# Performance work log

Measured on AMD Instinct MI355X. Metric: run time of the kernel, lower is better.

Reference implementation:

```python
import jax, jax.numpy as jnp
import numpy as np

B, T, D, H, O = 8, 16384, 256, 256, 256


def setup_inputs() -> dict:
    key = jax.random.key(0)
    ks = jax.random.split(key, 7)
    lim_d = 1.0 / np.sqrt(D)
    lim_h = 1.0 / np.sqrt(H)
    u = lambda k, shape, lim: jax.random.uniform(k, shape, jnp.float32, -lim, lim)
    return {
        "xs": jax.random.normal(ks[0], (B, T, D), jnp.float32),
        "Wz": u(ks[1], (H, D), lim_d),
        "bz": u(ks[2], (H,), lim_d),
        "Wh": u(ks[3], (H, D), lim_d),
        "bh": u(ks[4], (H,), lim_d),
        "Wo": u(ks[5], (O, H), lim_h),
        "bo": u(ks[6], (O,), lim_h),
    }


def reference(xs, Wz, bz, Wh, bh, Wo, bo):
    # gates and candidate hidden states (eqx.nn.Linear: y = W @ x + b)
    zs = jax.nn.sigmoid(jnp.einsum("btd,hd->bth", xs, Wz) + bz)  # [B,T,H]
    hs = jnp.einsum("btd,hd->bth", xs, Wh) + bh                  # [B,T,H]

    # prepend_ones / prepend_zeros along the time axis
    a = jnp.concatenate([jnp.ones_like(zs[:, :1]), 1.0 - zs], axis=1)    # [B,T+1,H]
    b = jnp.concatenate([jnp.zeros_like(zs[:, :1]), zs * hs], axis=1)    # [B,T+1,H]

    def combine(first, second):
        a0, b0 = first
        a1, b1 = second
        return (a0 * b0, b0 * a1 + b1)

    _, states = jax.lax.associative_scan(combine, (a, b), axis=1)
    return jnp.einsum("bth,oh->bto", states[:, 1:], Wo) + bo  # [B,T,O]
```

## Files before the change

### kernel.cpp

```cpp
#include <hip/hip_runtime.h>
#include <hip/hip_bf16.h>

#define Bsz 8
#define Tsz 16384
#define NL0 16385
#define NL5 512
#define NL10 16

typedef __attribute__((ext_vector_type(2))) float f32x2;
typedef __attribute__((ext_vector_type(4))) float f32x4;
typedef __attribute__((ext_vector_type(8))) short bf16x8;

__device__ __forceinline__ short f2bf(float f) {
  unsigned u = __builtin_bit_cast(unsigned, f);
  u += 0x7FFFu + ((u >> 16) & 1u);
  return (short)(u >> 16);
}
__device__ __forceinline__ unsigned cvtpk(float lo, float hi) {
  __hip_bfloat162 t = __float22bfloat162_rn(float2{lo, hi});
  unsigned u;
  __builtin_memcpy(&u, &t, 4);
  return u;
}
__device__ __forceinline__ bf16x8 pack8(f32x4 a, f32x4 b) {
  union { unsigned u[4]; bf16x8 v; } r;
  r.u[0] = cvtpk(a[0], a[1]); r.u[1] = cvtpk(a[2], a[3]);
  r.u[2] = cvtpk(b[0], b[1]); r.u[3] = cvtpk(b[2], b[3]);
  return r.v;
}
__device__ __forceinline__ void unpk(unsigned u, float& a, float& b) {
  a = __builtin_bit_cast(float, u << 16);
  b = __builtin_bit_cast(float, u & 0xFFFF0000u);
}

__global__ void fill_sentinel(float* __restrict__ out, int n) {
  int i = blockIdx.x * blockDim.x + threadIdx.x;
  if (i < n) out[i] = 12345.0f;
}

__global__ void prep_weights(const float* __restrict__ Wz, const float* __restrict__ Wh,
                             const float* __restrict__ Wo, unsigned short* __restrict__ wt) {
  int idx = blockIdx.x * 256 + threadIdx.x;
  if (idx >= 3 * 256 * 32) return;
  int m   = idx >> 13;
  int rem = idx & 8191;
  int r   = rem >> 5;
  int cq  = rem & 31;
  const float* src = (m == 0 ? Wz : (m == 1 ? Wh : Wo)) + r * 256 + cq * 8;
  f32x4 v0 = *(const f32x4*)src;
  f32x4 v1 = *(const f32x4*)(src + 4);
  *(bf16x8*)(wt + m * 65536 + (cq * 256 + r) * 8) = pack8(v0, v1);
}

__global__ void init_e0(unsigned* __restrict__ l0) {
  int idx = blockIdx.x * 256 + threadIdx.x;
  if (idx >= Bsz * 256) return;
  int batch = idx >> 8, h = idx & 255;
  l0[(size_t)batch * NL0 * 256 + h] = 0x00003F80u;
}

__global__ __launch_bounds__(512, 4)
void gemm_zh(const float* __restrict__ xs, const unsigned short* __restrict__ wt,
             const float* __restrict__ bz, const float* __restrict__ bh,
             unsigned* __restrict__ l0)
{
  __shared__ __align__(16) unsigned short aL[32][64][8];

  const int tid = threadIdx.x;
  const int wave = tid >> 6, lane = tid & 63, l15 = lane & 15, l4 = lane >> 4;
  const int rowBase = blockIdx.x * 64;
  const int srow = tid & 63, soct = tid >> 6;
  const float* aptr = xs + (size_t)(rowBase + srow) * 256 + soct * 8;
  const unsigned short* wz_t = wt;
  const unsigned short* wh_t = wt + 65536;
  const int wn = wave * 32;

  {
    f32x4 avA[4], avB[4];
#pragma unroll
    for (int q = 0; q < 4; ++q) {
      avA[q] = *(const f32x4*)(aptr + q * 64);
      avB[q] = *(const f32x4*)(aptr + q * 64 + 4);
    }
#pragma unroll
    for (int q = 0; q < 4; ++q)
      *(bf16x8*)&aL[soct + q * 8][srow][0] = pack8(avA[q], avB[q]);
  }
  __syncthreads();

  f32x4 accz[4][2] = {};
  f32x4 acch[4][2] = {};

  bf16x8 zc[2], hc[2], zn[2], hn[2];
#pragma unroll
  for (int n = 0; n < 2; ++n) {
    const int r = wn + n * 16 + l15;
    zc[n] = *(const bf16x8*)(wz_t + (l4 * 256 + r) * 8);
    hc[n] = *(const bf16x8*)(wh_t + (l4 * 256 + r) * 8);
  }

#pragma unroll
  for (int kk = 0; kk < 8; ++kk) {
    if (kk < 7) {
      const int cq = (kk + 1) * 4 + l4;
#pragma unroll
      for (int n = 0; n < 2; ++n) {
        const int r = wn + n * 16 + l15;
        zn[n] = *(const bf16x8*)(wz_t + (cq * 256 + r) * 8);
        hn[n] = *(const bf16x8*)(wh_t + (cq * 256 + r) * 8);
      }
    }
    bf16x8 af[4];
#pragma unroll
    for (int m = 0; m < 4; ++m)
      af[m] = *(const bf16x8*)&aL[kk * 4 + l4][m * 16 + l15][0];
#pragma unroll
    for (int m = 0; m < 4; ++m)
#pragma unroll
      for (int n = 0; n < 2; ++n) {
        accz[m][n] = __builtin_amdgcn_mfma_f32_16x16x32_bf16(af[m], zc[n], accz[m][n], 0, 0, 0);
        acch[m][n] = __builtin_amdgcn_mfma_f32_16x16x32_bf16(af[m], hc[n], acch[m][n], 0, 0, 0);
      }
    if (kk < 7) {
      zc[0] = zn[0]; zc[1] = zn[1];
      hc[0] = hn[0]; hc[1] = hn[1];
    }
  }

  const int batch = rowBase >> 14;
  const int tRow  = rowBase & (Tsz - 1);
#pragma unroll
  for (int n = 0; n < 2; ++n) {
    const int col = wn + n * 16 + l15;
    const float bzv = bz[col], bhv = bh[col];
#pragma unroll
    for (int m = 0; m < 4; ++m)
#pragma unroll
      for (int j = 0; j < 4; ++j) {
        const int t = tRow + m * 16 + l4 * 4 + j;
        const float zv = 1.0f / (1.0f + __expf(-(accz[m][n][j] + bzv)));
        const float hv = acch[m][n][j] + bhv;
        l0[((size_t)batch * NL0 + t + 1) * 256 + col] = cvtpk(1.0f - zv, zv * hv);
      }
  }
}

__global__ __launch_bounds__(256)
void chunk_up_bf16(const unsigned* __restrict__ l0, f32x2* __restrict__ dst)
{
  int idx = blockIdx.x * 256 + threadIdx.x;
  int h2 = idx & 127, r = idx >> 7;
  int c = r & 511, batch = r >> 9;
  size_t base = ((size_t)batch * NL0 + (size_t)c * 32) * 256 + h2 * 2;

  float ax[16], bx[16], ay[16], by[16];
#pragma unroll
  for (int i = 0; i < 16; ++i) {
    uint2 e0 = *(const uint2*)(l0 + base + (size_t)(2 * i) * 256);
    uint2 e1 = *(const uint2*)(l0 + base + (size_t)(2 * i + 1) * 256);
    float a0, b0, a1, b1;
    unpk(e0.x, a0, b0); unpk(e1.x, a1, b1);
    ax[i] = a0 * b0; bx[i] = b0 * a1 + b1;
    unpk(e0.y, a0, b0); unpk(e1.y, a1, b1);
    ay[i] = a0 * b0; by[i] = b0 * a1 + b1;
  }
#pragma unroll
  for (int n = 8; n >= 1; n >>= 1) {
#pragma unroll
    for (int i = 0; i < n; ++i) {
      float nax = ax[2*i] * bx[2*i], nbx = bx[2*i] * ax[2*i+1] + bx[2*i+1];
      float nay = ay[2*i] * by[2*i], nby = by[2*i] * ay[2*i+1] + by[2*i+1];
      ax[i] = nax; bx[i] = nbx; ay[i] = nay; by[i] = nby;
    }
  }
  f32x4 o = {ax[0], bx[0], ay[0], by[0]};
  *(f32x4*)((float*)dst + (((size_t)batch * 512 + c) * 256 + h2 * 2) * 2) = o;
}

__global__ __launch_bounds__(256)
void chunk_up(const f32x2* __restrict__ src, f32x2* __restrict__ dst, int nCh, int nSrc)
{
  int idx = blockIdx.x * 256 + threadIdx.x;
  int total = Bsz * nCh * 256;
  if (idx >= total) return;
  int h = idx & 255, r = idx >> 8;
  int c = r % nCh, batch = r / nCh;
  size_t base = ((size_t)batch * nSrc + (size_t)c * 32) * 256 + h;

  float a1[16], b1[16];
#pragma unroll
  for (int i = 0; i < 16; ++i) {
    f32x2 e0 = src[base + (size_t)(2 * i) * 256];
    f32x2 e1 = src[base + (size_t)(2 * i + 1) * 256];
    a1[i] = e0[0] * e0[1];
    b1[i] = e0[1] * e1[0] + e1[1];
  }
#pragma unroll
  for (int n = 8; n >= 1; n >>= 1) {
#pragma unroll
    for (int i = 0; i < n; ++i) {
      float na = a1[2 * i] * b1[2 * i];
      float nb = b1[2 * i] * a1[2 * i + 1] + b1[2 * i + 1];
      a1[i] = na; b1[i] = nb;
    }
  }
  dst[((size_t)batch * nCh + c) * 256 + h] = f32x2{a1[0], b1[0]};
}

__global__ void tree16(const f32x2* __restrict__ src, float* __restrict__ outB)
{
  int idx = blockIdx.x * 256 + threadIdx.x;
  if (idx >= Bsz * 256) return;
  int h = idx & 255, batch = idx >> 8;
  size_t base = (size_t)batch * 16 * 256 + h;

  float a0[16], b0[16];
#pragma unroll
  for (int i = 0; i < 16; ++i) { f32x2 e = src[base + (size_t)i * 256]; a0[i] = e[0]; b0[i] = e[1]; }
  float a1[8], b1[8];
#pragma unroll
  for (int i = 0; i < 8; ++i) { a1[i] = a0[2*i]*b0[2*i]; b1[i] = b0[2*i]*a0[2*i+1] + b0[2*i+1]; }
  float a2[4], b2[4];
#pragma unroll
  for (int i = 0; i < 4; ++i) { a2[i] = a1[2*i]*b1[2*i]; b2[i] = b1[2*i]*a1[2*i+1] + b1[2*i+1]; }
  float a3[2], b3[2];
#pragma unroll
  for (int i = 0; i < 2; ++i) { a3[i] = a2[2*i]*b2[2*i]; b3[i] = b2[2*i]*a2[2*i+1] + b2[2*i+1]; }
  float s3[2];
  s3[0] = b3[0];
  s3[1] = b3[0] * a3[1] + b3[1];
  float s2[4];
  s2[0] = b2[0]; s2[1] = s3[0]; s2[2] = s3[0] * a2[2] + b2[2]; s2[3] = s3[1];
  float s1[8];
  s1[0] = b1[0];
#pragma unroll
  for (int j = 0; j < 4; ++j) s1[2*j+1] = s2[j];
#pragma unroll
  for (int j = 1; j < 4; ++j) s1[2*j] = s2[j-1] * a1[2*j] + b1[2*j];
  float s0[16];
  s0[0] = b0[0];
#pragma unroll
  for (int j = 0; j < 8; ++j) s0[2*j+1] = s1[j];
#pragma unroll
  for (int j = 1; j < 8; ++j) s0[2*j] = s1[j-1] * a0[2*j] + b0[2*j];
#pragma unroll
  for (int i = 0; i < 16; ++i) outB[base + (size_t)i * 256] = s0[i];
}

__global__ __launch_bounds__(256, 2)
void chunk_down_f32(const f32x2* __restrict__ src, const float* __restrict__ snext,
                    float* __restrict__ outF, int nCh, int nFull, int nSrc)
{
  int idx = blockIdx.x * 256 + threadIdx.x;
  int total = Bsz * nCh * 256;
  if (idx >= total) return;
  int h = idx & 255, r = idx >> 8;
  int c = r % nCh, batch = r / nCh;
  size_t base = ((size_t)batch * nSrc + (size_t)c * 32) * 256 + h;
  bool hasP = (c > 0);
  float P = hasP ? snext[((size_t)batch * nFull + (c - 1)) * 256 + h] : 0.0f;
  float S = snext[((size_t)batch * nFull + c) * 256 + h];

  float ae[16], be[16], a1[16], b1[16];
#pragma unroll
  for (int i = 0; i < 16; ++i) {
    f32x2 e0 = src[base + (size_t)(2 * i) * 256];
    f32x2 e1 = src[base + (size_t)(2 * i + 1) * 256];
    ae[i] = e0[0]; be[i] = e0[1];
    a1[i] = e0[0] * e0[1];
    b1[i] = e0[1] * e1[0] + e1[1];
  }
  float a2[8], b2[8];
#pragma unroll
  for (int i = 0; i < 8; ++i) { a2[i] = a1[2*i]*b1[2*i]; b2[i] = b1[2*i]*a1[2*i+1] + b1[2*i+1]; }
  float a3[4], b3[4];
#pragma unroll
  for (int i = 0; i < 4; ++i) { a3[i] = a2[2*i]*b2[2*i]; b3[i] = b2[2*i]*a2[2*i+1] + b2[2*i+1]; }
  float a4[2], b4[2];
#pragma unroll
  for (int i = 0; i < 2; ++i) { a4[i] = a3[2*i]*b3[2*i]; b4[i] = b3[2*i]*a3[2*i+1] + b3[2*i+1]; }

  float s4[2];
  s4[0] = hasP ? P * a4[0] + b4[0] : b4[0];
  s4[1] = S;
  float s3[4];
  s3[0] = hasP ? P * a3[0] + b3[0] : b3[0];
  s3[1] = s4[0]; s3[2] = s4[0] * a3[2] + b3[2]; s3[3] = s4[1];
  float s2[8];
  s2[0] = hasP ? P * a2[0] + b2[0] : b2[0];
#pragma unroll
  for (int j = 0; j < 4; ++j) s2[2*j+1] = s3[j];
#pragma unroll
  for (int j = 1; j < 4; ++j) s2[2*j] = s3[j-1] * a2[2*j] + b2[2*j];
  float s1[16];
  s1[0] = hasP ? P * a1[0] + b1[0] : b1[0];
#pragma unroll
  for (int j = 0; j < 8; ++j) s1[2*j+1] = s2[j];
#pragma unroll
  for (int j = 1; j < 8; ++j) s1[2*j] = s2[j-1] * a1[2*j] + b1[2*j];

  outF[base] = hasP ? P * ae[0] + be[0] : be[0];
#pragma unroll
  for (int j = 0; j < 16; ++j) outF[base + (size_t)(2*j+1) * 256] = s1[j];
#pragma unroll
  for (int j = 1; j < 16; ++j) outF[base + (size_t)(2*j) * 256] = s1[j-1] * ae[j] + be[j];
}

__global__ __launch_bounds__(256, 2)
void down_proj(const unsigned* __restrict__ l0, const float* __restrict__ s5b,
               const unsigned short* __restrict__ wo_t, const float* __restrict__ bo,
               float* __restrict__ out)
{
  __shared__ unsigned short pL[32 * 256];

  const int tid = threadIdx.x;
  const int bc = blockIdx.x;
  const int c = bc % 513;
  const int batch = bc / 513;

  {
    const int h = tid;
    const size_t base = ((size_t)batch * NL0 + (size_t)c * 32) * 256 + h;
    const bool hasP = (c > 0);
    const float P = hasP ? s5b[((size_t)batch * 512 + (c - 1)) * 256 + h] : 0.0f;

    if (c == 512) {
      float a0, b0; unpk(l0[base], a0, b0);
      pL[h] = (unsigned short)f2bf(P * a0 + b0);
#pragma unroll
      for (int i = 1; i < 32; ++i)
        pL[i * 256 + (h ^ ((i & 7) << 3))] = 0;
    } else {
      const float S = s5b[((size_t)batch * 512 + c) * 256 + h];
      float ae[16], be[16], a1[16], b1[16];
#pragma unroll
      for (int i = 0; i < 16; ++i) {
        unsigned u0 = l0[base + (size_t)(2 * i) * 256];
        unsigned u1 = l0[base + (size_t)(2 * i + 1) * 256];
        float a0, b0, a1e, b1e;
        unpk(u0, a0, b0); unpk(u1, a1e, b1e);
        ae[i] = a0; be[i] = b0;
        a1[i] = a0 * b0; b1[i] = b0 * a1e + b1e;
      }
      float a2[8], b2[8];
#pragma unroll
      for (int i = 0; i < 8; ++i) { a2[i] = a1[2*i]*b1[2*i]; b2[i] = b1[2*i]*a1[2*i+1] + b1[2*i+1]; }
      float a3[4], b3[4];
#pragma unroll
      for (int i = 0; i < 4; ++i) { a3[i] = a2[2*i]*b2[2*i]; b3[i] = b2[2*i]*a2[2*i+1] + b2[2*i+1]; }
      float a4[2], b4[2];
#pragma unroll
      for (int i = 0; i < 2; ++i) { a4[i] = a3[2*i]*b3[2*i]; b4[i] = b3[2*i]*a3[2*i+1] + b3[2*i+1]; }

      float s4[2];
      s4[0] = hasP ? P * a4[0] + b4[0] : b4[0];
      s4[1] = S;
      float s3[4];
      s3[0] = hasP ? P * a3[0] + b3[0] : b3[0];
      s3[1] = s4[0]; s3[2] = s4[0] * a3[2] + b3[2]; s3[3] = s4[1];
      float s2[8];
      s2[0] = hasP ? P * a2[0] + b2[0] : b2[0];
#pragma unroll
      for (int j = 0; j < 4; ++j) s2[2*j+1] = s3[j];
#pragma unroll
      for (int j = 1; j < 4; ++j) s2[2*j] = s3[j-1] * a2[2*j] + b2[2*j];
      float s1[16];
      s1[0] = hasP ? P * a1[0] + b1[0] : b1[0];
#pragma unroll
      for (int j = 0; j < 8; ++j) s1[2*j+1] = s2[j];
#pragma unroll
      for (int j = 1; j < 8; ++j) s1[2*j] = s2[j-1] * a1[2*j] + b1[2*j];

      pL[h] = (unsigned short)f2bf(hasP ? P * ae[0] + be[0] : be[0]);
#pragma unroll
      for (int j = 0; j < 16; ++j) {
        const int row = 2 * j + 1;
        pL[row * 256 + (h ^ ((row & 7) << 3))] = (unsigned short)f2bf(s1[j]);
      }
#pragma unroll
      for (int j = 1; j < 16; ++j) {
        const int row = 2 * j;
        pL[row * 256 + (h ^ ((row & 7) << 3))] = (unsigned short)f2bf(s1[j-1] * ae[j] + be[j]);
      }
    }
  }
  __syncthreads();

  const int wave = tid >> 6, lane = tid & 63, l15 = lane & 15, l4 = lane >> 4;
  const int wn = wave * 64;
  f32x4 acc[2][4] = {};
  bf16x8 wc[4], wnx[4];
#pragma unroll
  for (int n = 0; n < 4; ++n)
    wc[n] = *(const bf16x8*)(wo_t + (l4 * 256 + wn + n * 16 + l15) * 8);
#pragma unroll
  for (int kk = 0; kk < 8; ++kk) {
    if (kk < 7) {
#pragma unroll
      for (int n = 0; n < 4; ++n)
        wnx[n] = *(const bf16x8*)(wo_t + (((kk + 1) * 4 + l4) * 256 + wn + n * 16 + l15) * 8);
    }
    bf16x8 af[2];
#pragma unroll
    for (int m = 0; m < 2; ++m) {
      const int row = m * 16 + l15;
      af[m] = *(const bf16x8*)&pL[row * 256 + ((kk * 32 + l4 * 8) ^ ((row & 7) << 3))];
    }
#pragma unroll
    for (int m = 0; m < 2; ++m)
#pragma unroll
      for (int n = 0; n < 4; ++n)
        acc[m][n] = __builtin_amdgcn_mfma_f32_16x16x32_bf16(af[m], wc[n], acc[m][n], 0, 0, 0);
    if (kk < 7) {
      wc[0] = wnx[0]; wc[1] = wnx[1]; wc[2] = wnx[2]; wc[3] = wnx[3];
    }
  }

  const int tBase = 32 * c - 1;
#pragma unroll
  for (int n = 0; n < 4; ++n) {
    const int col = wn + n * 16 + l15;
    const float bv = bo[col];
#pragma unroll
    for (int m = 0; m < 2; ++m)
#pragma unroll
      for (int j = 0; j < 4; ++j) {
        const int t = tBase + m * 16 + l4 * 4 + j;
        if ((unsigned)t < (unsigned)Tsz)
          out[((size_t)batch * Tsz + t) * 256 + col] = acc[m][n][j] + bv;
      }
  }
}

extern "C" void kernel_launch(void* const* d_in, const int* in_sizes, int n_in,
                              void* d_out, int out_size, void* d_ws, size_t ws_size,
                              hipStream_t stream)
{
  (void)in_sizes; (void)n_in;
  const float* xs = (const float*)d_in[0];
  const float* Wz = (const float*)d_in[1];
  const float* bz = (const float*)d_in[2];
  const float* Wh = (const float*)d_in[3];
  const float* bh = (const float*)d_in[4];
  const float* Wo = (const float*)d_in[5];
  const float* bo = (const float*)d_in[6];
  float* out = (float*)d_out;

  const size_t n_l0  = (size_t)Bsz * NL0 * 256;
  const size_t n_l5  = (size_t)Bsz * NL5 * 256;
  const size_t n_l10 = (size_t)Bsz * NL10 * 256;

  unsigned* l0    = (unsigned*)d_ws;
  f32x2* l5ab     = (f32x2*)(l0 + n_l0);
  f32x2* l10ab    = l5ab + n_l5;
  float* s10b     = (float*)(l10ab + n_l10);
  float* s5b      = s10b + n_l10;
  unsigned short* wt = (unsigned short*)(s5b + n_l5);

  const size_t need = n_l0 * 4 + n_l5 * 8 + n_l10 * 8 + n_l10 * 4 + n_l5 * 4 + 3 * 65536 * 2;
  if (ws_size < need) {
    fill_sentinel<<<(out_size + 255) / 256, 256, 0, stream>>>(out, out_size);
    return;
  }

  prep_weights<<<96, 256, 0, stream>>>(Wz, Wh, Wo, wt);
  init_e0<<<8, 256, 0, stream>>>(l0);
  gemm_zh<<<Bsz * Tsz / 64, 512, 0, stream>>>(xs, wt, bz, bh, l0);

  chunk_up_bf16<<<(Bsz * 512 * 128) / 256, 256, 0, stream>>>(l0, l5ab);
  chunk_up<<<(Bsz * 16 * 256) / 256, 256, 0, stream>>>(l5ab, l10ab, 16, NL5);
  tree16<<<8, 256, 0, stream>>>(l10ab, s10b);
  chunk_down_f32<<<(Bsz * 16 * 256) / 256, 256, 0, stream>>>(l5ab, s10b, s5b, 16, 16, NL5);

  down_proj<<<Bsz * 513, 256, 0, stream>>>(l0, s5b, wt + 2 * 65536, bo, out);
}
```

Baseline: 186.4 us.

## Retile gemm_zh to 32-row blocks with 4 waves, swizzled LDS and coalesced loads

The gate/candidate GEMM now uses 32-row tiles with 256 threads, and each wave covers 64 output columns instead of 32. The xs tile is loaded with contiguous per-thread addresses and stored to LDS with an XOR swizzle to avoid bank conflicts. The register double-buffering of weight fragments is dropped in favour of loading them each k-step. This halves A-tile reuse per weight fragment, so weight traffic from L2 doubles, in exchange for more blocks and better coalescing of the xs load.

```diff
diff --git a/kernel.cpp b/kernel.cpp
--- a/kernel.cpp
+++ b/kernel.cpp
@@ -59,82 +59,73 @@
   l0[(size_t)batch * NL0 * 256 + h] = 0x00003F80u;
 }
 
-__global__ __launch_bounds__(512, 4)
+__global__ __launch_bounds__(256, 2)
 void gemm_zh(const float* __restrict__ xs, const unsigned short* __restrict__ wt,
              const float* __restrict__ bz, const float* __restrict__ bh,
              unsigned* __restrict__ l0)
 {
-  __shared__ __align__(16) unsigned short aL[32][64][8];
+  __shared__ __align__(16) unsigned short aL[32][32][8];
 
   const int tid = threadIdx.x;
   const int wave = tid >> 6, lane = tid & 63, l15 = lane & 15, l4 = lane >> 4;
-  const int rowBase = blockIdx.x * 64;
-  const int srow = tid & 63, soct = tid >> 6;
-  const float* aptr = xs + (size_t)(rowBase + srow) * 256 + soct * 8;
+  const int rowBase = blockIdx.x * 32;
+  const float* base = xs + (size_t)rowBase * 256;
   const unsigned short* wz_t = wt;
   const unsigned short* wh_t = wt + 65536;
-  const int wn = wave * 32;
+  const int wn = wave * 64;
 
   {
-    f32x4 avA[4], avB[4];
-#pragma unroll
-    for (int q = 0; q < 4; ++q) {
-      avA[q] = *(const f32x4*)(aptr + q * 64);
-      avB[q] = *(const f32x4*)(aptr + q * 64 + 4);
-    }
-#pragma unroll
-    for (int q = 0; q < 4; ++q)
-      *(bf16x8*)&aL[soct + q * 8][srow][0] = pack8(avA[q], avB[q]);
+    f32x4 av0[4], av1[4];
+#pragma unroll
+    for (int k = 0; k < 4; ++k) {
+      av0[k] = *(const f32x4*)(base + tid * 8 + k * 2048);
+      av1[k] = *(const f32x4*)(base + tid * 8 + k * 2048 + 4);
+    }
+#pragma unroll
+    for (int k = 0; k < 4; ++k) {
+      const int o = tid + k * 256;
+      const int row = o >> 5, oct = o & 31;
+      *(bf16x8*)&aL[row][oct ^ (row & 7)][0] = pack8(av0[k], av1[k]);
+    }
   }
   __syncthreads();
 
-  f32x4 accz[4][2] = {};
-  f32x4 acch[4][2] = {};
-
-  bf16x8 zc[2], hc[2], zn[2], hn[2];
-#pragma unroll
-  for (int n = 0; n < 2; ++n) {
-    const int r = wn + n * 16 + l15;
-    zc[n] = *(const bf16x8*)(wz_t + (l4 * 256 + r) * 8);
-    hc[n] = *(const bf16x8*)(wh_t + (l4 * 256 + r) * 8);
-  }
+  f32x4 accz[2][4] = {};
+  f32x4 acch[2][4] = {};
 
 #pragma unroll
   for (int kk = 0; kk < 8; ++kk) {
-    if (kk < 7) {
-      const int cq = (kk + 1) * 4 + l4;
-#pragma unroll
-      for (int n = 0; n < 2; ++n) {
-        const int r = wn + n * 16 + l15;
-        zn[n] = *(const bf16x8*)(wz_t + (cq * 256 + r) * 8);
-        hn[n] = *(const bf16x8*)(wh_t + (cq * 256 + r) * 8);
-      }
-    }
-    bf16x8 af[4];
-#pragma unroll
-    for (int m = 0; m < 4; ++m)
-      af[m] = *(const bf16x8*)&aL[kk * 4 + l4][m * 16 + l15][0];
-#pragma unroll
-    for (int m = 0; m < 4; ++m)
-#pragma unroll
-      for (int n = 0; n < 2; ++n) {
-        accz[m][n] = __builtin_amdgcn_mfma_f32_16x16x32_bf16(af[m], zc[n], accz[m][n], 0, 0, 0);
-        acch[m][n] = __builtin_amdgcn_mfma_f32_16x16x32_bf16(af[m], hc[n], acch[m][n], 0, 0, 0);
-      }
-    if (kk < 7) {
-      zc[0] = zn[0]; zc[1] = zn[1];
-      hc[0] = hn[0]; hc[1] = hn[1];
-    }
+    bf16x8 af[2];
+#pragma unroll
+    for (int m = 0; m < 2; ++m) {
+      const int row = m * 16 + l15;
+      af[m] = *(const bf16x8*)&aL[row][(kk * 4 + l4) ^ (row & 7)][0];
+    }
+    const int cq = kk * 4 + l4;
+    bf16x8 zf[4], hf[4];
+#pragma unroll
+    for (int n = 0; n < 4; ++n) {
+      const int r = wn + n * 16 + l15;
+      zf[n] = *(const bf16x8*)(wz_t + (cq * 256 + r) * 8);
+      hf[n] = *(const bf16x8*)(wh_t + (cq * 256 + r) * 8);
+    }
+#pragma unroll
+    for (int m = 0; m < 2; ++m)
+#pragma unroll
+      for (int n = 0; n < 4; ++n) {
+        accz[m][n] = __builtin_amdgcn_mfma_f32_16x16x32_bf16(af[m], zf[n], accz[m][n], 0, 0, 0);
+        acch[m][n] = __builtin_amdgcn_mfma_f32_16x16x32_bf16(af[m], hf[n], acch[m][n], 0, 0, 0);
+      }
   }
 
   const int batch = rowBase >> 14;
   const int tRow  = rowBase & (Tsz - 1);
 #pragma unroll
-  for (int n = 0; n < 2; ++n) {
+  for (int n = 0; n < 4; ++n) {
     const int col = wn + n * 16 + l15;
     const float bzv = bz[col], bhv = bh[col];
 #pragma unroll
-    for (int m = 0; m < 4; ++m)
+    for (int m = 0; m < 2; ++m)
 #pragma unroll
       for (int j = 0; j < 4; ++j) {
         const int t = tRow + m * 16 + l4 * 4 + j;
@@ -465,7 +456,7 @@
 
   prep_weights<<<96, 256, 0, stream>>>(Wz, Wh, Wo, wt);
   init_e0<<<8, 256, 0, stream>>>(l0);
-  gemm_zh<<<Bsz * Tsz / 64, 512, 0, stream>>>(xs, wt, bz, bh, l0);
+  gemm_zh<<<Bsz * Tsz / 32, 256, 0, stream>>>(xs, wt, bz, bh, l0);
 
   chunk_up_bf16<<<(Bsz * 512 * 128) / 256, 256, 0, stream>>>(l0, l5ab);
   chunk_up<<<(Bsz * 16 * 256) / 256, 256, 0, stream>>>(l5ab, l10ab, 16, NL5);
```

Result: no change. 183.7 us (-1.5%).
